# Performance work log

Hardware: AMD Instinct MI355X
Metric: run time of the kernel (lower is better)

Reference implementation:

```python
import jax, jax.numpy as jnp
import numpy as np

D = 1024
H = 16
B = 4
S = 2048
NEG = -1000000000.0


def setup_inputs() -> dict:
    key = jax.random.key(0)
    ks = jax.random.split(key, 12)
    s = 0.02
    inp = {
        "Q": jax.random.normal(ks[0], (B, S, D), jnp.float32),
        "K": jax.random.normal(ks[1], (B, S, D), jnp.float32),
        "V": jax.random.normal(ks[2], (B, S, D), jnp.float32),
        # causal mask, broadcastable to [B, H, S, S]
        "mask": jnp.broadcast_to(jnp.tril(jnp.ones((S, S), bool)), (B, 1, S, S)),
        "Wq": jax.random.normal(ks[3], (D, D), jnp.float32) * s,
        "bq": jnp.zeros((D,), jnp.float32),
        "Wk": jax.random.normal(ks[4], (D, D), jnp.float32) * s,
        "bk": jnp.zeros((D,), jnp.float32),
        "Wv": jax.random.normal(ks[5], (D, D), jnp.float32) * s,
        "bv": jnp.zeros((D,), jnp.float32),
        "Wo": jax.random.normal(ks[6], (D, D), jnp.float32) * s,
        "bo": jnp.zeros((D,), jnp.float32),
    }
    return inp


def reference(Q, K, V, mask, Wq, bq, Wk, bk, Wv, bv, Wo, bo):
    d = D // H  # head dim
    def split(x):  # [B,S,D] -> [B,H,S,d]
        Bx, Sx, _ = x.shape
        return x.reshape(Bx, Sx, H, d).transpose(0, 2, 1, 3)

    q = split(Q @ Wq + bq)
    k = split(K @ Wk + bk)
    v = split(V @ Wv + bv)

    scores = jnp.einsum("bhsd,bhtd->bhst", q, k) / jnp.sqrt(jnp.float32(d))
    scores = jnp.where(mask, scores, NEG)
    attn = jax.nn.softmax(scores, axis=-1)
    out = jnp.einsum("bhst,bhtd->bhsd", attn, v)  # [B,H,S,d]
    out = out.transpose(0, 2, 1, 3).reshape(Q.shape[0], Q.shape[1], D)
    return out @ Wo + bo
```

## Files before the change

kernel.cpp:

```cpp
#include <hip/hip_runtime.h>
#include <hip/hip_bf16.h>
#include <type_traits>

#define DEV __device__ __forceinline__

typedef short bf16x8 __attribute__((ext_vector_type(8)));
typedef float f32x4 __attribute__((ext_vector_type(4)));
typedef float f32x16 __attribute__((ext_vector_type(16)));
typedef unsigned u32x4 __attribute__((ext_vector_type(4)));

static DEV unsigned short f2bf(float f) {
  unsigned u = __builtin_bit_cast(unsigned, f);
  u += 0x7FFFu + ((u >> 16) & 1u);
  return (unsigned short)(u >> 16);
}

static DEV unsigned cvtpk(float lo, float hi) {
  unsigned d;
  asm("v_cvt_pk_bf16_f32 %0, %1, %2" : "=v"(d) : "v"(lo), "v"(hi));
  return d;
}

static DEV void pl32(unsigned& x, unsigned& y) {
  asm("v_permlane32_swap_b32 %0, %1" : "+v"(x), "+v"(y));
}

static DEV void gl_lds16(const void* g, void* l) {
  __builtin_amdgcn_global_load_lds(
      (const __attribute__((address_space(1))) unsigned*)g,
      (__attribute__((address_space(3))) unsigned*)l, 16, 0, 0);
}

#define QSCALE 0.18033688f

__global__ __launch_bounds__(256) void wtrans4(const float* __restrict__ W0,
                                               const float* __restrict__ W1,
                                               const float* __restrict__ W2,
                                               const float* __restrict__ W3,
                                               unsigned short* __restrict__ T0,
                                               unsigned short* __restrict__ T1,
                                               unsigned short* __restrict__ T2,
                                               unsigned short* __restrict__ T3) {
  const int z = blockIdx.z;
  const float* W = z == 0 ? W0 : z == 1 ? W1 : z == 2 ? W2 : W3;
  unsigned short* Wt = z == 0 ? T0 : z == 1 ? T1 : z == 2 ? T2 : T3;
  const float wsc = (z == 0) ? QSCALE : 1.0f;
  __shared__ __align__(16) unsigned short T[64][72];
  const int tid = threadIdx.x;
  const int k0 = blockIdx.x * 64, n0 = blockIdx.y * 64;
  const int r = tid >> 4, c4 = (tid & 15) * 4;
  for (int j = 0; j < 4; ++j) {
    int row = j * 16 + r;
    float4 v = *(const float4*)&W[(size_t)(k0 + row) * 1024 + n0 + c4];
    ushort4 w;
    w.x = f2bf(v.x * wsc); w.y = f2bf(v.y * wsc);
    w.z = f2bf(v.z * wsc); w.w = f2bf(v.w * wsc);
    *(ushort4*)&T[row][c4] = w;
  }
  __syncthreads();
  for (int j = 0; j < 4; ++j) {
    int n = j * 16 + r;
    ushort4 w;
    w.x = T[c4 + 0][n]; w.y = T[c4 + 1][n]; w.z = T[c4 + 2][n]; w.w = T[c4 + 3][n];
    *(ushort4*)&Wt[(size_t)(n0 + n) * 1024 + k0 + c4] = w;
  }
}

template <typename InT, typename OutT, bool TRANSV>
DEV void gemm_lds_body(unsigned short* SMG, const InT* __restrict__ X,
                       const unsigned short* __restrict__ Wt,
                       const float* __restrict__ bias, OutT* __restrict__ Y,
                       float bsc) {
  constexpr bool AF32 = std::is_same_v<InT, float>;
  const int tid = threadIdx.x, lane = tid & 63, wid = tid >> 6;
  const int id = blockIdx.y * 64 + blockIdx.x;
  const int xcd = id & 7, jj = id >> 3;
  const int m0 = (xcd * 8 + (jj & 7)) * 128;
  const int n0 = (jj >> 3) * 128;
  const int wm = (wid >> 1) * 64, wn = (wid & 1) * 64;
  f32x4 acc[4][4] = {};

  const int srow = wid * 32 + (lane >> 3);
  const int scol = (((lane & 7) ^ ((lane >> 3) & 7))) * 8;
  const unsigned short* gB = &Wt[(size_t)(n0 + srow) * 1024 + scol];
  const unsigned short* gAb = nullptr;
  const float* gAf = nullptr;
  float4 aF[8];

#define ABUF(P) (SMG + (P)*16384)
#define BBUF(P) (SMG + (P)*16384 + 8192)
#define DSWRITE_A(P)                                                              \
  do {                                                                            \
    _Pragma("unroll") for (int q = 0; q < 4; ++q) {                               \
      uint4 w;                                                                    \
      w.x = cvtpk(aF[2 * q].x, aF[2 * q].y);                                      \
      w.y = cvtpk(aF[2 * q].z, aF[2 * q].w);                                      \
      w.z = cvtpk(aF[2 * q + 1].x, aF[2 * q + 1].y);                              \
      w.w = cvtpk(aF[2 * q + 1].z, aF[2 * q + 1].w);                              \
      *(uint4*)&ABUF(P)[(srow + q * 8) * 64 + scol] = w;                          \
    }                                                                             \
  } while (0)
#define LOAD_AF(K0)                                                               \
  do {                                                                            \
    _Pragma("unroll") for (int q = 0; q < 4; ++q) {                               \
      aF[2 * q] = *(const float4*)(gAf + (size_t)q * 8192 + (K0));                \
      aF[2 * q + 1] = *(const float4*)(gAf + (size_t)q * 8192 + (K0) + 4);        \
    }                                                                             \
  } while (0)

  if constexpr (AF32) {
    gAf = &X[(size_t)(m0 + srow) * 1024 + (lane & 7) * 8];
    LOAD_AF(0);
    DSWRITE_A(0);
    LOAD_AF(64);
  } else {
    gAb = &X[(size_t)(m0 + srow) * 1024 + scol];
#pragma unroll
    for (int q = 0; q < 4; ++q)
      gl_lds16(gAb + (size_t)q * 8192, &ABUF(0)[wid * 32 * 64] + q * 8 * 64);
  }
#pragma unroll
  for (int q = 0; q < 4; ++q)
    gl_lds16(gB + (size_t)q * 8192, &BBUF(0)[wid * 32 * 64] + q * 8 * 64);
  __syncthreads();

  for (int t = 0; t < 16; ++t) {
    const int p = t & 1;
    if (t + 1 < 16) {
      const int kn = (t + 1) * 64;
#pragma unroll
      for (int q = 0; q < 4; ++q)
        gl_lds16(gB + (size_t)q * 8192 + kn, &BBUF(p ^ 1)[wid * 32 * 64] + q * 8 * 64);
      if constexpr (AF32) {
        DSWRITE_A(p ^ 1);
      } else {
#pragma unroll
        for (int q = 0; q < 4; ++q)
          gl_lds16(gAb + (size_t)q * 8192 + kn, &ABUF(p ^ 1)[wid * 32 * 64] + q * 8 * 64);
      }
    }
    __builtin_amdgcn_sched_barrier(0);
    if constexpr (AF32) {
      if (t + 2 < 16) LOAD_AF((t + 2) * 64);
    }
    const unsigned short* Asp = ABUF(p);
    const unsigned short* Bsp = BBUF(p);
#pragma unroll
    for (int kk = 0; kk < 2; ++kk) {
      const int kb = ((kk * 4 + (lane >> 4)) ^ (lane & 7)) * 8;
      bf16x8 af[4], bfr[4];
#pragma unroll
      for (int i = 0; i < 4; ++i)
        af[i] = *(const bf16x8*)&Asp[(wm + i * 16 + (lane & 15)) * 64 + kb];
#pragma unroll
      for (int i = 0; i < 4; ++i)
        bfr[i] = *(const bf16x8*)&Bsp[(wn + i * 16 + (lane & 15)) * 64 + kb];
      __builtin_amdgcn_s_setprio(1);
#pragma unroll
      for (int mi = 0; mi < 4; ++mi)
#pragma unroll
        for (int ni = 0; ni < 4; ++ni)
          acc[mi][ni] =
              __builtin_amdgcn_mfma_f32_16x16x32_bf16(af[mi], bfr[ni], acc[mi][ni], 0, 0, 0);
      __builtin_amdgcn_s_setprio(0);
    }
    __syncthreads();
  }
#undef LOAD_AF
#undef DSWRITE_A
#undef ABUF
#undef BBUF

  if constexpr (TRANSV) {
    const int bt = m0 >> 11;
    const int s0 = m0 & 2047;
    const int h0 = n0 >> 6;
    unsigned short* Tl = SMG;
#pragma unroll
    for (int cch = 0; cch < 2; ++cch) {
      __syncthreads();
      if ((wid >> 1) == cch) {
#pragma unroll
        for (int ni = 0; ni < 4; ++ni) {
          const int n = wn + ni * 16 + (lane & 15);
          const float bv = bias[n0 + n] * bsc;
#pragma unroll
          for (int mi = 0; mi < 4; ++mi) {
            const int mloc = mi * 16 + (lane >> 4) * 4;
#pragma unroll
            for (int r = 0; r < 4; r += 2) {
              const unsigned pk = cvtpk(acc[mi][ni][r] + bv, acc[mi][ni][r + 1] + bv);
              *(unsigned*)&Tl[n * 72 + mloc + r] = pk;
            }
          }
        }
      }
      __syncthreads();
      const int m8 = (tid & 7) * 8;
#pragma unroll
      for (int it = 0; it < 4; ++it) {
        const int nr = (tid >> 3) + it * 32;
        const int h = h0 + (nr >> 6), dv = nr & 63;
        uint4 v = *(const uint4*)&Tl[nr * 72 + m8];
        *(uint4*)&((unsigned short*)Y)[(((size_t)bt * 16 + h) * 64 + dv) * 2048 +
                                       s0 + cch * 64 + m8] = v;
      }
    }
  } else {
    for (int ni = 0; ni < 4; ++ni) {
      const int col = n0 + wn + ni * 16 + (lane & 15);
      const float bv = bias[col] * bsc;
      for (int mi = 0; mi < 4; ++mi) {
        const int row = m0 + wm + mi * 16 + (lane >> 4) * 4;
        for (int r = 0; r < 4; ++r) {
          float v = acc[mi][ni][r] + bv;
          if constexpr (std::is_same_v<OutT, float>)
            Y[(size_t)(row + r) * 1024 + col] = v;
          else
            Y[(size_t)(row + r) * 1024 + col] = f2bf(v);
        }
      }
    }
  }
}

__global__ __launch_bounds__(256) void gemm_qkv3(
    const float* __restrict__ X0, const float* __restrict__ X1,
    const float* __restrict__ X2, const unsigned short* __restrict__ W0,
    const unsigned short* __restrict__ W1, const unsigned short* __restrict__ W2,
    const float* __restrict__ b0, const float* __restrict__ b1,
    const float* __restrict__ b2, unsigned short* __restrict__ Y0,
    unsigned short* __restrict__ Y1, unsigned short* __restrict__ Y2) {
  __shared__ __align__(16) unsigned short SMG[32768];
  const int z = blockIdx.z;
  const float* X = z == 0 ? X0 : z == 1 ? X1 : X2;
  const unsigned short* Wt = z == 0 ? W0 : z == 1 ? W1 : W2;
  const float* bias = z == 0 ? b0 : z == 1 ? b1 : b2;
  unsigned short* Y = z == 0 ? Y0 : z == 1 ? Y1 : Y2;
  if (z == 2)
    gemm_lds_body<float, unsigned short, true>(SMG, X, Wt, bias, Y, 1.0f);
  else
    gemm_lds_body<float, unsigned short, false>(SMG, X, Wt, bias, Y,
                                                z == 0 ? QSCALE : 1.0f);
}

__global__ __launch_bounds__(256) void gemm_out(const unsigned short* __restrict__ X,
                                                const unsigned short* __restrict__ Wt,
                                                const float* __restrict__ bias,
                                                float* __restrict__ Y) {
  __shared__ __align__(16) unsigned short SMG[32768];
  gemm_lds_body<unsigned short, float, false>(SMG, X, Wt, bias, Y, 1.0f);
}

__global__ __launch_bounds__(256) void attn_fwd(const unsigned short* __restrict__ Qb,
                                                const unsigned short* __restrict__ Kb,
                                                const unsigned short* __restrict__ Vt,
                                                unsigned short* __restrict__ Ob) {
  constexpr int KP = 72;
  __shared__ __align__(16) unsigned short SM[4 * 64 * KP];
  const int tid = threadIdx.x, lane = tid & 63, wid = tid >> 6;
  const int l31 = lane & 31, hi = lane >> 5;
  const int id = blockIdx.x;
  const int xcd = id & 7, idx = id >> 3;
  const int bh = xcd + 8 * (idx & 7);
  const int qb = idx >> 3;
  const int q0 = (15 - qb) * 128;
  const int b = bh >> 4, h = bh & 15;
  const size_t rowbase = (size_t)b * 2048;
  const int col0 = h * 64;
  const int qmin = q0 + wid * 32;
  const int myq = qmin + l31;
  const unsigned short* Vrow = Vt + (size_t)bh * 64 * 2048;
  const int rr = tid >> 3, c8 = (tid & 7) * 8;

  bf16x8 qf[4];
#pragma unroll
  for (int c = 0; c < 4; ++c)
    qf[c] = *(const bf16x8*)&Qb[(rowbase + myq) * 1024 + col0 + c * 16 + hi * 8];

  const bf16x8 onesv =
      __builtin_bit_cast(bf16x8, (u32x4){0x3F803F80u, 0x3F803F80u, 0x3F803F80u, 0x3F803F80u});

  f32x16 o[2], rsa;
  o[0] = 0.f; o[1] = 0.f; rsa = 0.f;

  const int NT = q0 / 64 + 2;
  uint4 kr0, kr1, vr0, vr1;
#define LOADT(KV0)                                                              \
  do {                                                                          \
    const int _k = (KV0);                                                       \
    kr0 = *(const uint4*)&Kb[(rowbase + _k + rr) * 1024 + col0 + c8];           \
    kr1 = *(const uint4*)&Kb[(rowbase + _k + rr + 32) * 1024 + col0 + c8];      \
    vr0 = *(const uint4*)&Vrow[(size_t)rr * 2048 + _k + c8];                    \
    vr1 = *(const uint4*)&Vrow[(size_t)(rr + 32) * 2048 + _k + c8];             \
  } while (0)

  LOADT(0);
  {
    unsigned short* Ks = SM;
    unsigned short* Vs = SM + 64 * KP;
    *(uint4*)&Ks[rr * KP + c8] = kr0;
    *(uint4*)&Ks[(rr + 32) * KP + c8] = kr1;
    *(uint4*)&Vs[rr * KP + c8] = vr0;
    *(uint4*)&Vs[(rr + 32) * KP + c8] = vr1;
    LOADT(64);
    __syncthreads();
  }

  for (int t = 0; t < NT; ++t) {
    const int kv0 = t * 64;
    const int p = t & 1;
    if (kv0 <= qmin + 31) {
      const unsigned short* Ks = SM + p * 128 * KP;
      const unsigned short* Vs = Ks + 64 * KP;

      f32x16 s2[2];
      s2[0] = 0.f; s2[1] = 0.f;
      __builtin_amdgcn_s_setprio(1);
#pragma unroll
      for (int m = 0; m < 2; ++m)
#pragma unroll
        for (int c = 0; c < 4; ++c) {
          bf16x8 kf = *(const bf16x8*)&Ks[(m * 32 + l31) * KP + c * 16 + hi * 8];
          s2[m] = __builtin_amdgcn_mfma_f32_32x32x16_bf16(kf, qf[c], s2[m], 0, 0, 0);
        }
      __builtin_amdgcn_s_setprio(0);

      if (kv0 + 63 > qmin) {
        const int thr = l31 + (qmin - kv0);
#pragma unroll
        for (int m = 0; m < 2; ++m)
#pragma unroll
          for (int r = 0; r < 16; ++r) {
            const int kvl = m * 32 + (r & 3) + 8 * (r >> 2) + 4 * hi;
            if (kvl > thr) s2[m][r] = -1.0e30f;
          }
      }

#pragma unroll
      for (int m = 0; m < 2; ++m)
#pragma unroll
        for (int r = 0; r < 16; ++r)
          s2[m][r] = __builtin_amdgcn_exp2f(s2[m][r]);

      bf16x8 pf[4];
#pragma unroll
      for (int m = 0; m < 2; ++m) {
        unsigned a0 = cvtpk(s2[m][0], s2[m][1]), a1 = cvtpk(s2[m][2], s2[m][3]);
        unsigned b0 = cvtpk(s2[m][4], s2[m][5]), b1 = cvtpk(s2[m][6], s2[m][7]);
        pl32(a0, b0);
        pl32(a1, b1);
        pf[2 * m] = __builtin_bit_cast(bf16x8, (u32x4){a0, a1, b0, b1});
        unsigned c0 = cvtpk(s2[m][8], s2[m][9]), c1 = cvtpk(s2[m][10], s2[m][11]);
        unsigned d0 = cvtpk(s2[m][12], s2[m][13]), d1 = cvtpk(s2[m][14], s2[m][15]);
        pl32(c0, d0);
        pl32(c1, d1);
        pf[2 * m + 1] = __builtin_bit_cast(bf16x8, (u32x4){c0, c1, d0, d1});
      }

      __builtin_amdgcn_s_setprio(1);
#pragma unroll
      for (int nt = 0; nt < 2; ++nt)
#pragma unroll
        for (int cc = 0; cc < 4; ++cc) {
          bf16x8 vf = *(const bf16x8*)&Vs[(nt * 32 + l31) * KP + cc * 16 + hi * 8];
          o[nt] = __builtin_amdgcn_mfma_f32_32x32x16_bf16(vf, pf[cc], o[nt], 0, 0, 0);
        }
#pragma unroll
      for (int cc = 0; cc < 4; ++cc)
        rsa = __builtin_amdgcn_mfma_f32_32x32x16_bf16(onesv, pf[cc], rsa, 0, 0, 0);
      __builtin_amdgcn_s_setprio(0);
    }
    if (t + 1 < NT) {
      unsigned short* Ks = SM + (p ^ 1) * 128 * KP;
      unsigned short* Vs = Ks + 64 * KP;
      *(uint4*)&Ks[rr * KP + c8] = kr0;
      *(uint4*)&Ks[(rr + 32) * KP + c8] = kr1;
      *(uint4*)&Vs[rr * KP + c8] = vr0;
      *(uint4*)&Vs[(rr + 32) * KP + c8] = vr1;
      if (t + 2 < NT) LOADT(kv0 + 128);
    }
    __syncthreads();
  }
#undef LOADT

  unsigned short* Os = SM + wid * 32 * KP;
  const float inv = 1.0f / rsa[0];
#pragma unroll
  for (int nt = 0; nt < 2; ++nt)
#pragma unroll
    for (int rq = 0; rq < 4; ++rq)
#pragma unroll
      for (int j = 0; j < 2; ++j) {
        const int r = rq * 4 + 2 * j;
        const unsigned pk = cvtpk(o[nt][r] * inv, o[nt][r + 1] * inv);
        *(unsigned*)&Os[l31 * KP + nt * 32 + 8 * rq + 4 * hi + 2 * j] = pk;
      }
  __syncthreads();
#pragma unroll
  for (int i = 0; i < 4; ++i) {
    const int qq = (lane >> 3) + i * 8;
    const int dvc = (lane & 7) * 8;
    uint4 val = *(const uint4*)&Os[qq * KP + dvc];
    *(uint4*)&Ob[(rowbase + qmin + qq) * 1024 + col0 + dvc] = val;
  }
}

extern "C" void kernel_launch(void* const* d_in, const int* in_sizes, int n_in,
                              void* d_out, int out_size, void* d_ws, size_t ws_size,
                              hipStream_t stream) {
  const float* Q  = (const float*)d_in[0];
  const float* K  = (const float*)d_in[1];
  const float* V  = (const float*)d_in[2];
  const float* Wq = (const float*)d_in[4];
  const float* bq = (const float*)d_in[5];
  const float* Wk = (const float*)d_in[6];
  const float* bk = (const float*)d_in[7];
  const float* Wv = (const float*)d_in[8];
  const float* bv = (const float*)d_in[9];
  const float* Wo = (const float*)d_in[10];
  const float* bo = (const float*)d_in[11];
  float* out = (float*)d_out;

  const size_t MB = 1024 * 1024;
  char* ws = (char*)d_ws;
  unsigned short* qb  = (unsigned short*)(ws + 0 * MB);
  unsigned short* kb  = (unsigned short*)(ws + 16 * MB);
  unsigned short* vtB = (unsigned short*)(ws + 32 * MB);
  unsigned short* ob  = (unsigned short*)(ws + 48 * MB);
  unsigned short* wtq = (unsigned short*)(ws + 64 * MB);
  unsigned short* wtk = (unsigned short*)(ws + 66 * MB);
  unsigned short* wtv = (unsigned short*)(ws + 68 * MB);
  unsigned short* wto = (unsigned short*)(ws + 70 * MB);

  wtrans4<<<dim3(16, 16, 4), 256, 0, stream>>>(Wq, Wk, Wv, Wo, wtq, wtk, wtv, wto);

  gemm_qkv3<<<dim3(64, 8, 3), 256, 0, stream>>>(Q, K, V, wtq, wtk, wtv,
                                                bq, bk, bv, qb, kb, vtB);

  attn_fwd<<<1024, 256, 0, stream>>>(qb, kb, vtB, ob);

  gemm_out<<<dim3(64, 8), 256, 0, stream>>>(ob, wto, bo, out);
}
```

Baseline: 171.0 us.

## Enlarge GEMM tiles to 256x128 with 512-thread blocks

The projection GEMMs now use 256-row by 128-column output tiles computed by eight waves. The B tile in LDS is shared across twice as many A rows, which cuts weight reloads, and the grid and staging indices are rewritten to match. The cost is more LDS per block (96 KB double-buffered), which lowers occupancy, and half as many blocks, which may underfill the CUs.

After: 165.3 us (median of 4 runs). 1.03x faster.

```diff
diff --git a/kernel.cpp b/kernel.cpp
--- a/kernel.cpp
+++ b/kernel.cpp
@@ -72,23 +72,26 @@
                        const float* __restrict__ bias, OutT* __restrict__ Y,
                        float bsc) {
   constexpr bool AF32 = std::is_same_v<InT, float>;
+  constexpr int HBUF = 24576;
   const int tid = threadIdx.x, lane = tid & 63, wid = tid >> 6;
-  const int id = blockIdx.y * 64 + blockIdx.x;
+  const int id = blockIdx.y * 32 + blockIdx.x;
   const int xcd = id & 7, jj = id >> 3;
-  const int m0 = (xcd * 8 + (jj & 7)) * 128;
-  const int n0 = (jj >> 3) * 128;
+  const int m0 = (xcd * 4 + (jj & 3)) * 256;
+  const int n0 = (jj >> 2) * 128;
   const int wm = (wid >> 1) * 64, wn = (wid & 1) * 64;
   f32x4 acc[4][4] = {};
 
-  const int srow = wid * 32 + (lane >> 3);
-  const int scol = (((lane & 7) ^ ((lane >> 3) & 7))) * 8;
-  const unsigned short* gB = &Wt[(size_t)(n0 + srow) * 1024 + scol];
+  const int srowA = tid >> 3;
+  const int slotA = ((tid & 7) ^ (srowA & 7)) * 8;
+  const int rB = wid * 16 + (lane >> 3);
+  const int scolB = (((lane & 7) ^ ((lane >> 3) & 7))) * 8;
+  const unsigned short* gB = &Wt[(size_t)(n0 + rB) * 1024 + scolB];
   const unsigned short* gAb = nullptr;
   const float* gAf = nullptr;
   float4 aF[8];
 
-#define ABUF(P) (SMG + (P)*16384)
-#define BBUF(P) (SMG + (P)*16384 + 8192)
+#define ABUF(P) (SMG + (P)*HBUF)
+#define BBUF(P) (SMG + (P)*HBUF + 16384)
 #define DSWRITE_A(P)                                                              \
   do {                                                                            \
     _Pragma("unroll") for (int q = 0; q < 4; ++q) {                               \
@@ -97,46 +100,50 @@
       w.y = cvtpk(aF[2 * q].z, aF[2 * q].w);                                      \
       w.z = cvtpk(aF[2 * q + 1].x, aF[2 * q + 1].y);                              \
       w.w = cvtpk(aF[2 * q + 1].z, aF[2 * q + 1].w);                              \
-      *(uint4*)&ABUF(P)[(srow + q * 8) * 64 + scol] = w;                          \
+      *(uint4*)&ABUF(P)[(srowA + q * 64) * 64 + slotA] = w;                       \
     }                                                                             \
   } while (0)
 #define LOAD_AF(K0)                                                               \
   do {                                                                            \
     _Pragma("unroll") for (int q = 0; q < 4; ++q) {                               \
-      aF[2 * q] = *(const float4*)(gAf + (size_t)q * 8192 + (K0));                \
-      aF[2 * q + 1] = *(const float4*)(gAf + (size_t)q * 8192 + (K0) + 4);        \
+      aF[2 * q] = *(const float4*)(gAf + (size_t)q * 65536 + (K0));               \
+      aF[2 * q + 1] = *(const float4*)(gAf + (size_t)q * 65536 + (K0) + 4);       \
     }                                                                             \
   } while (0)
+#define STAGE_B(P, K0)                                                            \
+  do {                                                                            \
+    _Pragma("unroll") for (int q = 0; q < 2; ++q)                                 \
+        gl_lds16(gB + (size_t)q * 8 * 1024 + (K0),                                \
+                 &BBUF(P)[(wid * 16 + q * 8) * 64]);                              \
+  } while (0)
+#define STAGE_AB16(P, K0)                                                         \
+  do {                                                                            \
+    _Pragma("unroll") for (int q = 0; q < 4; ++q)                                 \
+        gl_lds16(gAb + (size_t)q * 8 * 1024 + (K0),                               \
+                 &ABUF(P)[(wid * 32 + q * 8) * 64]);                              \
+  } while (0)
 
   if constexpr (AF32) {
-    gAf = &X[(size_t)(m0 + srow) * 1024 + (lane & 7) * 8];
+    gAf = &X[(size_t)(m0 + srowA) * 1024 + (tid & 7) * 8];
     LOAD_AF(0);
     DSWRITE_A(0);
     LOAD_AF(64);
   } else {
-    gAb = &X[(size_t)(m0 + srow) * 1024 + scol];
-#pragma unroll
-    for (int q = 0; q < 4; ++q)
-      gl_lds16(gAb + (size_t)q * 8192, &ABUF(0)[wid * 32 * 64] + q * 8 * 64);
-  }
-#pragma unroll
-  for (int q = 0; q < 4; ++q)
-    gl_lds16(gB + (size_t)q * 8192, &BBUF(0)[wid * 32 * 64] + q * 8 * 64);
+    gAb = &X[(size_t)(m0 + wid * 32 + (lane >> 3)) * 1024 + scolB];
+    STAGE_AB16(0, 0);
+  }
+  STAGE_B(0, 0);
   __syncthreads();
 
   for (int t = 0; t < 16; ++t) {
     const int p = t & 1;
     if (t + 1 < 16) {
       const int kn = (t + 1) * 64;
-#pragma unroll
-      for (int q = 0; q < 4; ++q)
-        gl_lds16(gB + (size_t)q * 8192 + kn, &BBUF(p ^ 1)[wid * 32 * 64] + q * 8 * 64);
+      STAGE_B(p ^ 1, kn);
       if constexpr (AF32) {
         DSWRITE_A(p ^ 1);
       } else {
-#pragma unroll
-        for (int q = 0; q < 4; ++q)
-          gl_lds16(gAb + (size_t)q * 8192 + kn, &ABUF(p ^ 1)[wid * 32 * 64] + q * 8 * 64);
+        STAGE_AB16(p ^ 1, kn);
       }
     }
     __builtin_amdgcn_sched_barrier(0);
@@ -168,6 +175,8 @@
   }
 #undef LOAD_AF
 #undef DSWRITE_A
+#undef STAGE_B
+#undef STAGE_AB16
 #undef ABUF
 #undef BBUF
 
@@ -177,7 +186,7 @@
     const int h0 = n0 >> 6;
     unsigned short* Tl = SMG;
 #pragma unroll
-    for (int cch = 0; cch < 2; ++cch) {
+    for (int cch = 0; cch < 4; ++cch) {
       __syncthreads();
       if ((wid >> 1) == cch) {
 #pragma unroll
@@ -198,8 +207,8 @@
       __syncthreads();
       const int m8 = (tid & 7) * 8;
 #pragma unroll
-      for (int it = 0; it < 4; ++it) {
-        const int nr = (tid >> 3) + it * 32;
+      for (int it = 0; it < 2; ++it) {
+        const int nr = (tid >> 3) + it * 64;
         const int h = h0 + (nr >> 6), dv = nr & 63;
         uint4 v = *(const uint4*)&Tl[nr * 72 + m8];
         *(uint4*)&((unsigned short*)Y)[(((size_t)bt * 16 + h) * 64 + dv) * 2048 +
@@ -224,14 +233,14 @@
   }
 }
 
-__global__ __launch_bounds__(256) void gemm_qkv3(
+__global__ __launch_bounds__(512) void gemm_qkv3(
     const float* __restrict__ X0, const float* __restrict__ X1,
     const float* __restrict__ X2, const unsigned short* __restrict__ W0,
     const unsigned short* __restrict__ W1, const unsigned short* __restrict__ W2,
     const float* __restrict__ b0, const float* __restrict__ b1,
     const float* __restrict__ b2, unsigned short* __restrict__ Y0,
     unsigned short* __restrict__ Y1, unsigned short* __restrict__ Y2) {
-  __shared__ __align__(16) unsigned short SMG[32768];
+  __shared__ __align__(16) unsigned short SMG[49152];
   const int z = blockIdx.z;
   const float* X = z == 0 ? X0 : z == 1 ? X1 : X2;
   const unsigned short* Wt = z == 0 ? W0 : z == 1 ? W1 : W2;
@@ -244,11 +253,11 @@
                                                 z == 0 ? QSCALE : 1.0f);
 }
 
-__global__ __launch_bounds__(256) void gemm_out(const unsigned short* __restrict__ X,
+__global__ __launch_bounds__(512) void gemm_out(const unsigned short* __restrict__ X,
                                                 const unsigned short* __restrict__ Wt,
                                                 const float* __restrict__ bias,
                                                 float* __restrict__ Y) {
-  __shared__ __align__(16) unsigned short SMG[32768];
+  __shared__ __align__(16) unsigned short SMG[49152];
   gemm_lds_body<unsigned short, float, false>(SMG, X, Wt, bias, Y, 1.0f);
 }
 
@@ -435,10 +444,10 @@
 
   wtrans4<<<dim3(16, 16, 4), 256, 0, stream>>>(Wq, Wk, Wv, Wo, wtq, wtk, wtv, wto);
 
-  gemm_qkv3<<<dim3(64, 8, 3), 256, 0, stream>>>(Q, K, V, wtq, wtk, wtv,
+  gemm_qkv3<<<dim3(32, 8, 3), 512, 0, stream>>>(Q, K, V, wtq, wtk, wtv,
                                                 bq, bk, bv, qb, kb, vtB);
 
   attn_fwd<<<1024, 256, 0, stream>>>(qb, kb, vtB, ob);
 
-  gemm_out<<<dim3(64, 8), 256, 0, stream>>>(ob, wto, bo, out);
-}
+  gemm_out<<<dim3(32, 8), 512, 0, stream>>>(ob, wto, bo, out);
+}
```
